# Kernel optimization log

Measured on AMD Instinct MI355X. Metric: run time of the kernel, lower is better.

The kernel has to match this reference:

```python
import jax, jax.numpy as jnp
import numpy as np

HIDDEN = 1024
HEADS = 16
BATCH = 2
SEQ = 2048
# dropout_p = 0.1 but module evaluated in eval mode (training=False) -> identity


def setup_inputs() -> dict:
    key = jax.random.key(0)
    k1, k2, k3 = jax.random.split(key, 3)
    x = jax.random.normal(k1, (BATCH, SEQ, HIDDEN), dtype=jnp.float32)
    # unit-scaling Linear: weight ~ N(0,1) (reset_parameters uses nn.init.normal_)
    w_qkv = jax.random.normal(k2, (3 * HIDDEN, HIDDEN), dtype=jnp.float32)
    w_o = jax.random.normal(k3, (HIDDEN, HIDDEN), dtype=jnp.float32)
    return {"x": x, "w_qkv": w_qkv, "w_o": w_o}


def reference(x, w_qkv, w_o):
    b, s, hid = x.shape
    heads = HEADS
    d = hid // heads
    # unit-scaled linear (constraint='to_output_scale'): y = x @ W.T * fan_in**-0.5
    qkv = (x @ w_qkv.T) * (hid ** -0.5)            # [b, s, 3*hid]
    # einops 'b s (z h d) -> z b h s d'
    qkv = qkv.reshape(b, s, 3, heads, d)
    q = jnp.transpose(qkv[:, :, 0], (0, 2, 1, 3))   # [b, h, s, d]
    k = jnp.transpose(qkv[:, :, 1], (0, 2, 1, 3))
    v = jnp.transpose(qkv[:, :, 2], (0, 2, 1, 3))
    # unit-scaled matmul: scale = inner_dim**-0.5
    scores = jnp.einsum('bhqd,bhkd->bhqk', q, k) * (d ** -0.5)  # [b, h, s, s]
    # unit-scaled softmax: output_scale = n / sqrt(n - 1)
    attn = jax.nn.softmax(scores, axis=-1) * (s / np.sqrt(s - 1.0))
    # dropout inactive (eval mode)
    out = jnp.einsum('bhqk,bhkd->bhqd', attn, v) * (s ** -0.5)  # inner dim = s
    out = jnp.transpose(out, (0, 2, 1, 3)).reshape(b, s, hid)   # 'b h s d -> b s (h d)'
    return (out @ w_o.T) * (hid ** -0.5)
```

## Files before the change

kernel.cpp:

```cpp
#include <hip/hip_runtime.h>

typedef unsigned short u16;
typedef _Float16 f16x8 __attribute__((ext_vector_type(8)));
typedef _Float16 f16x4 __attribute__((ext_vector_type(4)));
typedef _Float16 f16x2 __attribute__((ext_vector_type(2)));
typedef float f32x4 __attribute__((ext_vector_type(4)));
typedef unsigned short u16x4 __attribute__((ext_vector_type(4)));

#define HID 1024
#define SEQ 2048
#define NH 16
#define DH 64

__device__ __forceinline__ u16 f2h(float f) {
  return __builtin_bit_cast(u16, (_Float16)f);
}
__device__ __forceinline__ f32x4 mfma_h(f16x8 a, f16x8 b, f32x4 c) {
  return __builtin_amdgcn_mfma_f32_16x16x32_f16(a, b, c, 0, 0, 0);
}
__device__ __forceinline__ float fexp2(float x) {
#if __has_builtin(__builtin_amdgcn_exp2f)
  return __builtin_amdgcn_exp2f(x);
#else
  return __expf(0.69314718f * x);
#endif
}
__device__ __forceinline__ f16x2 pkrtz(float a, float b) {
  return __builtin_bit_cast(f16x2, __builtin_amdgcn_cvt_pkrtz(a, b));
}
__device__ __forceinline__ void g2l16(const u16* g, u16* l) {
  __builtin_amdgcn_global_load_lds(
      (const __attribute__((address_space(1))) unsigned int*)g,
      (__attribute__((address_space(3))) unsigned int*)l, 16, 0, 0);
}

#define NX4 ((4096 * 1024) / 4)
#define NQ4 ((3072 * 1024) / 4)
#define NO4 ((1024 * 1024) / 4)
__global__ __launch_bounds__(256) void prep_kernel(
    const float* __restrict__ x, const float* __restrict__ wq,
    const float* __restrict__ wo,
    u16* __restrict__ x16, u16* __restrict__ wq16, u16* __restrict__ wo16) {
  int i = blockIdx.x * 256 + threadIdx.x;
  const float4 v = (i < NX4) ? ((const float4*)x)[i]
                 : (i < NX4 + NQ4) ? ((const float4*)wq)[i - NX4]
                 : ((const float4*)wo)[i - NX4 - NQ4];
  u16* dst = (i < NX4) ? &x16[(size_t)i * 4]
           : (i < NX4 + NQ4) ? &wq16[(size_t)(i - NX4) * 4]
           : &wo16[(size_t)(i - NX4 - NQ4) * 4];
  u16x4 o;
  o[0] = f2h(v.x); o[1] = f2h(v.y); o[2] = f2h(v.z); o[3] = f2h(v.w);
  *(u16x4*)dst = o;
}

__global__ __launch_bounds__(256, 3) void gemm_qkv(
    const u16* __restrict__ a16, const u16* __restrict__ b16,
    u16* __restrict__ qf, u16* __restrict__ kf, u16* __restrict__ vtf) {
  __shared__ __align__(16) u16 la[2][128 * 32], lb[2][128 * 32];
  const int t = threadIdx.x;
  const int lane = t & 63, w = t >> 6;
  const int wr = w >> 1, wc = w & 1;
  const int lr = lane & 15, lg = lane >> 4;
  const int br = blockIdx.x, bc = blockIdx.y;
  const f32x4 fzero = {0.f, 0.f, 0.f, 0.f};
  f32x4 acc[4][4];
#pragma unroll
  for (int i = 0; i < 4; ++i)
#pragma unroll
    for (int j = 0; j < 4; ++j) acc[i][j] = fzero;
  const int srow = t >> 2, scol = ((t & 3) ^ (srow & 3)) << 3;
  const u16* ga = a16 + (size_t)(br * 128 + srow) * HID + scol;
  const u16* gb = b16 + (size_t)(bc * 128 + srow) * HID + scol;
  const int lo16 = t * 8;

#define QSTAGE(buf, s)                                        \
  {                                                           \
    const int kk = (s) * 32;                                  \
    g2l16(ga + kk, &la[buf][lo16]);                           \
    g2l16(ga + kk + (size_t)64 * HID, &la[buf][lo16 + 2048]); \
    g2l16(gb + kk, &lb[buf][lo16]);                           \
    g2l16(gb + kk + (size_t)64 * HID, &lb[buf][lo16 + 2048]); \
  }

  QSTAGE(0, 0)
  for (int s = 0; s < 32; ++s) {
    const int cur = s & 1;
    __syncthreads();
    if (s + 1 < 32) QSTAGE(cur ^ 1, s + 1)
    f16x8 ah[4], bh[4];
#pragma unroll
    for (int i = 0; i < 4; ++i) {
      int row = wr * 64 + i * 16 + lr;
      ah[i] = *(const f16x8*)&la[cur][row * 32 + ((lg ^ (row & 3)) << 3)];
    }
#pragma unroll
    for (int j = 0; j < 4; ++j) {
      int row = wc * 64 + j * 16 + lr;
      bh[j] = *(const f16x8*)&lb[cur][row * 32 + ((lg ^ (row & 3)) << 3)];
    }
#pragma unroll
    for (int i = 0; i < 4; ++i)
#pragma unroll
      for (int j = 0; j < 4; ++j) acc[i][j] = mfma_h(ah[i], bh[j], acc[i][j]);
  }
#undef QSTAGE

  const int m0 = br * 128 + wr * 64;
  const int b = m0 >> 11, sbase = m0 & 2047;
  const int hcol = bc * 2 + wc;
  const int z = hcol >> 4, hh = hcol & 15;
  const int bhid = b * NH + hh;
  if (z == 2) {
#pragma unroll
    for (int i = 0; i < 4; ++i) {
      int s2b = sbase + ((i >> 1) << 5) + (lg << 3) + ((i & 1) << 2);
#pragma unroll
      for (int j = 0; j < 4; ++j) {
        int d = j * 16 + lr;
        u16x4 o;
#pragma unroll
        for (int r = 0; r < 4; ++r) o[r] = f2h(acc[i][j][r] * 0.03125f);
        *(u16x4*)&vtf[((size_t)bhid * DH + d) * SEQ + s2b] = o;
      }
    }
  } else {
    const float sc = (z == 0) ? 0.03125f * 0.18033688f : 0.03125f;
    u16* dst = (z == 0) ? qf : kf;
#pragma unroll
    for (int i = 0; i < 4; ++i)
#pragma unroll
      for (int j = 0; j < 4; ++j) {
        int d = j * 16 + lr;
#pragma unroll
        for (int r = 0; r < 4; ++r) {
          int ss = sbase + i * 16 + lg * 4 + r;
          dst[((size_t)bhid * SEQ + ss) * DH + d] = f2h(acc[i][j][r] * sc);
        }
      }
  }
}

__global__ __launch_bounds__(256, 2) void gemm_proj(
    const u16* __restrict__ po0, const u16* __restrict__ po1,
    const float* __restrict__ pl, const u16* __restrict__ b16,
    float* __restrict__ out) {
  __shared__ __align__(16) u16 la[128 * 64];
  __shared__ __align__(16) u16 lb[64 * 64];
  __shared__ float linv[16 * 128];
  const int t = threadIdx.x;
  const int lane = t & 63, w = t >> 6;
  const int wr = w >> 1, wc = w & 1;
  const int lr = lane & 15, lg = lane >> 4;
  const int br = blockIdx.x, bc = blockIdx.y;
  const f32x4 fzero = {0.f, 0.f, 0.f, 0.f};
  f32x4 acc[4][2];
#pragma unroll
  for (int i = 0; i < 4; ++i)
#pragma unroll
    for (int j = 0; j < 2; ++j) acc[i][j] = fzero;
#pragma unroll
  for (int jj = 0; jj < 8; ++jj) {
    int idx = t + jj * 256;
    int h = idx >> 7, i = idx & 127;
    int ar = br * 128 + i;
    int b = ar >> 11, s = ar & 2047;
    int bhs = (b * NH + h) * SEQ + s;
    linv[idx] = 1.00024426f / (pl[bhs] + pl[NH * 2 * SEQ + bhs]);
  }
  __syncthreads();
  const int srow = t >> 3, scol = ((t & 7) ^ (srow & 7)) << 3;
  const u16* gp0 = po0 + (size_t)(br * 128 + srow) * HID + scol;
  const u16* gp1 = po1 + (size_t)(br * 128 + srow) * HID + scol;
  const u16* gb = b16 + (size_t)(bc * 64 + srow) * HID + scol;
  const int lo16 = t * 8;
  for (int kk = 0; kk < HID; kk += 64) {
#pragma unroll
    for (int r = 0; r < 2; ++r)
      g2l16(gb + kk + (size_t)(r * 32) * HID, &lb[lo16 + r * 2048]);
#pragma unroll
    for (int r = 0; r < 4; ++r) {
      f16x8 a0 = *(const f16x8*)(gp0 + kk + (size_t)(r * 32) * HID);
      f16x8 a1 = *(const f16x8*)(gp1 + kk + (size_t)(r * 32) * HID);
      float invr = linv[((kk >> 6) << 7) + srow + r * 32];
      union { f16x2 h2[4]; f16x8 h8; } uo;
#pragma unroll
      for (int p = 0; p < 4; ++p) {
        float s0 = ((float)a0[2 * p] + (float)a1[2 * p]) * invr;
        float s1 = ((float)a0[2 * p + 1] + (float)a1[2 * p + 1]) * invr;
        uo.h2[p] = pkrtz(s0, s1);
      }
      *(f16x8*)&la[lo16 + r * 2048] = uo.h8;
    }
    __syncthreads();
#pragma unroll
    for (int ks = 0; ks < 2; ++ks) {
      f16x8 ah[4], bh[2];
#pragma unroll
      for (int i = 0; i < 4; ++i) {
        int row = wr * 64 + i * 16 + lr;
        ah[i] = *(const f16x8*)&la[row * 64 + (((ks * 4 + lg) ^ (row & 7)) << 3)];
      }
#pragma unroll
      for (int j = 0; j < 2; ++j) {
        int row = wc * 32 + j * 16 + lr;
        bh[j] = *(const f16x8*)&lb[row * 64 + (((ks * 4 + lg) ^ (row & 7)) << 3)];
      }
#pragma unroll
      for (int i = 0; i < 4; ++i)
#pragma unroll
        for (int j = 0; j < 2; ++j)
          acc[i][j] = mfma_h(ah[i], bh[j], acc[i][j]);
    }
    __syncthreads();
  }
  const int m0 = br * 128 + wr * 64, n0 = bc * 64 + wc * 32;
#pragma unroll
  for (int i = 0; i < 4; ++i)
#pragma unroll
    for (int j = 0; j < 2; ++j)
#pragma unroll
      for (int r = 0; r < 4; ++r) {
        int row = m0 + i * 16 + lg * 4 + r;
        int col = n0 + j * 16 + lr;
        out[(size_t)row * HID + col] = acc[i][j][r] * 0.03125f;
      }
}

__global__ __launch_bounds__(256, 4) void attn_kernel(
    const u16* __restrict__ qf, const u16* __restrict__ kf,
    const u16* __restrict__ vtf, u16* __restrict__ po0,
    u16* __restrict__ po1, float* __restrict__ pl) {
  __shared__ __align__(16) u16 lk[2][64 * 64];
  __shared__ __align__(16) u16 lv[2][64 * 64];
  const int t = threadIdx.x;
  const int lane = t & 63, w = t >> 6;
  const int lr = lane & 15, lg = lane >> 4;
  const int bh = blockIdx.x, qt = blockIdx.y, sp = blockIdx.z;
  const size_t base_qk = (size_t)bh * SEQ * DH;
  const size_t base_vt = (size_t)bh * DH * SEQ;

  f16x8 qfr[2][2];
#pragma unroll
  for (int rt = 0; rt < 2; ++rt)
#pragma unroll
    for (int ks = 0; ks < 2; ++ks)
      qfr[rt][ks] = *(const f16x8*)&qf[base_qk +
          (size_t)(qt * 128 + w * 32 + rt * 16 + lr) * DH + ks * 32 + lg * 8];

  f16x8 vones;
#pragma unroll
  for (int j = 0; j < 8; ++j) vones[j] = (_Float16)1.0f;

  const f32x4 fzero = {0.f, 0.f, 0.f, 0.f};
  f32x4 acc_o[2][4];
  f32x4 acc_l[2];
#pragma unroll
  for (int rt = 0; rt < 2; ++rt) {
    acc_l[rt] = fzero;
#pragma unroll
    for (int ct = 0; ct < 4; ++ct) acc_o[rt][ct] = fzero;
  }

  const int srow = t >> 3;
  const int scol = ((t & 7) ^ (srow & 7)) << 3;
  const int lo16 = t * 8;

  const u16* gk0 = kf + base_qk + (size_t)(sp * 1024 + srow) * DH + scol;
  const u16* gv0 = vtf + base_vt + (size_t)srow * SEQ + sp * 1024 + scol;

#define STAGE(buf, j)                                             \
  {                                                               \
    const u16* gk = gk0 + (size_t)(j) * 64 * DH;                  \
    g2l16(gk, &lk[buf][lo16]);                                    \
    g2l16(gk + 32 * DH, &lk[buf][lo16 + 2048]);                   \
    const u16* gv = gv0 + (j) * 64;                               \
    g2l16(gv, &lv[buf][lo16]);                                    \
    g2l16(gv + (size_t)32 * SEQ, &lv[buf][lo16 + 2048]);          \
  }

  STAGE(0, 0)

  for (int j = 0; j < 16; ++j) {
    const int cur = j & 1;
    __syncthreads();

    f32x4 sa[2][4];
    __builtin_amdgcn_s_setprio(1);
#pragma unroll
    for (int ct = 0; ct < 4; ++ct) {
      int row = ct * 16 + lr;
      f16x8 k0 = *(const f16x8*)&lk[cur][row * 64 + ((lg ^ (row & 7)) << 3)];
      f16x8 k1 = *(const f16x8*)&lk[cur][row * 64 + (((4 + lg) ^ (row & 7)) << 3)];
      sa[0][ct] = mfma_h(k0, qfr[0][0], fzero);
      sa[1][ct] = mfma_h(k0, qfr[1][0], fzero);
      sa[0][ct] = mfma_h(k1, qfr[0][1], sa[0][ct]);
      sa[1][ct] = mfma_h(k1, qfr[1][1], sa[1][ct]);
    }
    __builtin_amdgcn_s_setprio(0);

    if (j + 1 < 16) STAGE(cur ^ 1, j + 1)

    f16x8 pfr[2][2];
#pragma unroll
    for (int rt = 0; rt < 2; ++rt)
#pragma unroll
      for (int ks = 0; ks < 2; ++ks) {
        union { f16x2 h2[4]; f16x8 h8; } up;
#pragma unroll
        for (int hi = 0; hi < 2; ++hi) {
          float e0 = fexp2(sa[rt][ks * 2 + hi][0]);
          float e1 = fexp2(sa[rt][ks * 2 + hi][1]);
          float e2 = fexp2(sa[rt][ks * 2 + hi][2]);
          float e3 = fexp2(sa[rt][ks * 2 + hi][3]);
          up.h2[hi * 2] = pkrtz(e0, e1);
          up.h2[hi * 2 + 1] = pkrtz(e2, e3);
        }
        pfr[rt][ks] = up.h8;
      }

    __builtin_amdgcn_s_setprio(1);
#pragma unroll
    for (int ks = 0; ks < 2; ++ks)
#pragma unroll
      for (int ct = 0; ct < 4; ++ct) {
        int vrow = ct * 16 + lr;
        f16x8 vfr = *(const f16x8*)&lv[cur][vrow * 64 + (((ks * 4 + lg) ^ (vrow & 7)) << 3)];
#pragma unroll
        for (int rt = 0; rt < 2; ++rt) acc_o[rt][ct] = mfma_h(pfr[rt][ks], vfr, acc_o[rt][ct]);
      }
#pragma unroll
    for (int rt = 0; rt < 2; ++rt) {
      acc_l[rt] = mfma_h(pfr[rt][0], vones, acc_l[rt]);
      acc_l[rt] = mfma_h(pfr[rt][1], vones, acc_l[rt]);
    }
    __builtin_amdgcn_s_setprio(0);
  }

  const int b = bh >> 4, hh = bh & 15;
  u16* pob = sp ? po1 : po0;
  float* plb = pl + sp * (NH * 2 * SEQ);
#pragma unroll
  for (int rt = 0; rt < 2; ++rt)
#pragma unroll
    for (int r = 0; r < 4; ++r) {
      int s = qt * 128 + w * 32 + rt * 16 + lg * 4 + r;
      int row = b * SEQ + s;
      if (lr == 0) plb[bh * SEQ + s] = acc_l[rt][r];
#pragma unroll
      for (int ct = 0; ct < 4; ++ct) {
        int d = ct * 16 + lr;
        pob[(size_t)row * HID + hh * DH + d] = f2h(acc_o[rt][ct][r]);
      }
    }
}

extern "C" void kernel_launch(void* const* d_in, const int* in_sizes, int n_in,
                              void* d_out, int out_size, void* d_ws, size_t ws_size,
                              hipStream_t stream) {
  const float* x = (const float*)d_in[0];
  const float* w_qkv = (const float*)d_in[1];
  const float* w_o = (const float*)d_in[2];
  u16* ws = (u16*)d_ws;
  const size_t XS = (size_t)4096 * 1024;
  const size_t WQ = (size_t)3072 * 1024;
  const size_t WO = (size_t)1024 * 1024;
  u16* x16  = ws;           u16* wq16 = x16 + XS;
  u16* wo16 = wq16 + WQ;
  u16* q_f  = wo16 + WO;    u16* k_f  = q_f + XS;
  u16* vt_f = k_f + XS;     u16* po0  = vt_f + XS;
  u16* po1  = x16;
  float* pl = (float*)wq16;

  prep_kernel<<<(NX4 + NQ4 + NO4) / 256, 256, 0, stream>>>(
      x, w_qkv, w_o, x16, wq16, wo16);
  gemm_qkv<<<dim3(32, 24), 256, 0, stream>>>(x16, wq16, q_f, k_f, vt_f);
  attn_kernel<<<dim3(32, 16, 2), 256, 0, stream>>>(q_f, k_f, vt_f, po0, po1, pl);
  gemm_proj<<<dim3(32, 16), 256, 0, stream>>>(po0, po1, pl, wo16, (float*)d_out);
}
```

Before: 183.8 us.

## Double-buffer projection GEMM staging and change QKV LDS swizzle

```diff
diff --git a/kernel.cpp b/kernel.cpp
--- a/kernel.cpp
+++ b/kernel.cpp
@@ -68,7 +68,8 @@
   for (int i = 0; i < 4; ++i)
 #pragma unroll
     for (int j = 0; j < 4; ++j) acc[i][j] = fzero;
-  const int srow = t >> 2, scol = ((t & 3) ^ (srow & 3)) << 3;
+  const int srow = t >> 2;
+  const int scol = ((t & 3) ^ ((srow + (srow >> 2)) & 3)) << 3;
   const u16* ga = a16 + (size_t)(br * 128 + srow) * HID + scol;
   const u16* gb = b16 + (size_t)(bc * 128 + srow) * HID + scol;
   const int lo16 = t * 8;
@@ -91,12 +92,12 @@
 #pragma unroll
     for (int i = 0; i < 4; ++i) {
       int row = wr * 64 + i * 16 + lr;
-      ah[i] = *(const f16x8*)&la[cur][row * 32 + ((lg ^ (row & 3)) << 3)];
+      ah[i] = *(const f16x8*)&la[cur][row * 32 + ((lg ^ ((row + (row >> 2)) & 3)) << 3)];
     }
 #pragma unroll
     for (int j = 0; j < 4; ++j) {
       int row = wc * 64 + j * 16 + lr;
-      bh[j] = *(const f16x8*)&lb[cur][row * 32 + ((lg ^ (row & 3)) << 3)];
+      bh[j] = *(const f16x8*)&lb[cur][row * 32 + ((lg ^ ((row + (row >> 2)) & 3)) << 3)];
     }
 #pragma unroll
     for (int i = 0; i < 4; ++i)
@@ -144,8 +145,8 @@
     const u16* __restrict__ po0, const u16* __restrict__ po1,
     const float* __restrict__ pl, const u16* __restrict__ b16,
     float* __restrict__ out) {
-  __shared__ __align__(16) u16 la[128 * 64];
-  __shared__ __align__(16) u16 lb[64 * 64];
+  __shared__ __align__(16) u16 la[2][128 * 64];
+  __shared__ __align__(16) u16 lb[2][64 * 64];
   __shared__ float linv[16 * 128];
   const int t = threadIdx.x;
   const int lane = t & 63, w = t >> 6;
@@ -167,43 +168,65 @@
     int bhs = (b * NH + h) * SEQ + s;
     linv[idx] = 1.00024426f / (pl[bhs] + pl[NH * 2 * SEQ + bhs]);
   }
-  __syncthreads();
   const int srow = t >> 3, scol = ((t & 7) ^ (srow & 7)) << 3;
   const u16* gp0 = po0 + (size_t)(br * 128 + srow) * HID + scol;
   const u16* gp1 = po1 + (size_t)(br * 128 + srow) * HID + scol;
   const u16* gb = b16 + (size_t)(bc * 64 + srow) * HID + scol;
   const int lo16 = t * 8;
-  for (int kk = 0; kk < HID; kk += 64) {
-#pragma unroll
-    for (int r = 0; r < 2; ++r)
-      g2l16(gb + kk + (size_t)(r * 32) * HID, &lb[lo16 + r * 2048]);
-#pragma unroll
-    for (int r = 0; r < 4; ++r) {
-      f16x8 a0 = *(const f16x8*)(gp0 + kk + (size_t)(r * 32) * HID);
-      f16x8 a1 = *(const f16x8*)(gp1 + kk + (size_t)(r * 32) * HID);
-      float invr = linv[((kk >> 6) << 7) + srow + r * 32];
-      union { f16x2 h2[4]; f16x8 h8; } uo;
-#pragma unroll
-      for (int p = 0; p < 4; ++p) {
-        float s0 = ((float)a0[2 * p] + (float)a1[2 * p]) * invr;
-        float s1 = ((float)a0[2 * p + 1] + (float)a1[2 * p + 1]) * invr;
-        uo.h2[p] = pkrtz(s0, s1);
-      }
-      *(f16x8*)&la[lo16 + r * 2048] = uo.h8;
-    }
+  f16x8 a0[4], a1[4];
+
+#define PLOADA(s)                                                   \
+  {                                                                 \
+    const int kk = (s) * 64;                                        \
+    _Pragma("unroll") for (int r = 0; r < 4; ++r) {                 \
+      a0[r] = *(const f16x8*)(gp0 + kk + (size_t)(r * 32) * HID);   \
+      a1[r] = *(const f16x8*)(gp1 + kk + (size_t)(r * 32) * HID);   \
+    }                                                               \
+  }
+#define PSTAGEB(buf, s)                                             \
+  {                                                                 \
+    const int kk = (s) * 64;                                        \
+    g2l16(gb + kk, &lb[buf][lo16]);                                 \
+    g2l16(gb + kk + (size_t)32 * HID, &lb[buf][lo16 + 2048]);       \
+  }
+#define PCOMBINE(buf, s)                                            \
+  {                                                                 \
+    _Pragma("unroll") for (int r = 0; r < 4; ++r) {                 \
+      float invr = linv[((s) << 7) + srow + r * 32];                \
+      union { f16x2 h2[4]; f16x8 h8; } uo;                          \
+      _Pragma("unroll") for (int p = 0; p < 4; ++p) {               \
+        float s0 = ((float)a0[r][2 * p] + (float)a1[r][2 * p]) * invr;        \
+        float s1 = ((float)a0[r][2 * p + 1] + (float)a1[r][2 * p + 1]) * invr;\
+        uo.h2[p] = pkrtz(s0, s1);                                   \
+      }                                                             \
+      *(f16x8*)&la[buf][lo16 + r * 2048] = uo.h8;                   \
+    }                                                               \
+  }
+
+  __syncthreads();
+  PLOADA(0)
+  PSTAGEB(0, 0)
+  PCOMBINE(0, 0)
+
+  for (int s = 0; s < 16; ++s) {
+    const int cur = s & 1;
     __syncthreads();
+    if (s + 1 < 16) {
+      PLOADA(s + 1)
+      PSTAGEB(cur ^ 1, s + 1)
+    }
 #pragma unroll
     for (int ks = 0; ks < 2; ++ks) {
       f16x8 ah[4], bh[2];
 #pragma unroll
       for (int i = 0; i < 4; ++i) {
         int row = wr * 64 + i * 16 + lr;
-        ah[i] = *(const f16x8*)&la[row * 64 + (((ks * 4 + lg) ^ (row & 7)) << 3)];
+        ah[i] = *(const f16x8*)&la[cur][row * 64 + (((ks * 4 + lg) ^ (row & 7)) << 3)];
       }
 #pragma unroll
       for (int j = 0; j < 2; ++j) {
         int row = wc * 32 + j * 16 + lr;
-        bh[j] = *(const f16x8*)&lb[row * 64 + (((ks * 4 + lg) ^ (row & 7)) << 3)];
+        bh[j] = *(const f16x8*)&lb[cur][row * 64 + (((ks * 4 + lg) ^ (row & 7)) << 3)];
       }
 #pragma unroll
       for (int i = 0; i < 4; ++i)
@@ -211,8 +234,12 @@
         for (int j = 0; j < 2; ++j)
           acc[i][j] = mfma_h(ah[i], bh[j], acc[i][j]);
     }
-    __syncthreads();
-  }
+    if (s + 1 < 16) PCOMBINE(cur ^ 1, s + 1)
+  }
+#undef PLOADA
+#undef PSTAGEB
+#undef PCOMBINE
+
   const int m0 = br * 128 + wr * 64, n0 = bc * 64 + wc * 32;
 #pragma unroll
   for (int i = 0; i < 4; ++i)
```

New measurement: 179.9 us. -2.1%, faster.
